# Performance work log

Measured on AMD Instinct MI355X. Metric: run time of the kernel, lower is better.

## Reference

```python
import jax, jax.numpy as jnp
import numpy as np

B, SEQ, NF = 16, 512, 32
E, HID, PRED = 128, 512, 96
N_FFT, HOP, TOPM = 64, 32, 32
W = SEQ // HOP + 1          # 17 windows (centered STFT)
F = N_FFT // 2 + 1          # 33 onesided freqs
LAM = 0.01                  # sparsity_threshold (softshrink)
SCALE = 0.02


def _hann(n):
    # periodic hann, matches torch.hann_window default
    return 0.5 - 0.5 * jnp.cos(2.0 * jnp.pi * jnp.arange(n) / n)


def _softshrink(v):
    return jnp.sign(v) * jnp.maximum(jnp.abs(v) - LAM, 0.0)


def setup_inputs():
    key = jax.random.key(0)
    ks = jax.random.split(key, 12)
    d = {}
    d['x'] = jax.random.normal(ks[0], (B, SEQ, NF), jnp.float32)
    d['embeddings'] = jax.random.normal(ks[1], (1, E), jnp.float32)
    for nm, k in zip(['Wr', 'Wi', 'Wrl', 'Wil', 'Wrr', 'Wir'], ks[2:8]):
        d[nm] = SCALE * jax.random.normal(k, (W, E, E), jnp.float32)
    d['br'] = SCALE * jax.random.normal(ks[8], (W, E), jnp.float32)
    d['bi'] = SCALE * jax.random.normal(ks[9], (W, E), jnp.float32)
    d['fc_w1'] = SCALE * jax.random.normal(ks[10], (SEQ * E, HID), jnp.float32)
    d['fc_b1'] = jnp.zeros((HID,), jnp.float32)
    d['fc_w2'] = SCALE * jax.random.normal(ks[11], (HID, PRED), jnp.float32)
    d['fc_b2'] = jnp.zeros((PRED,), jnp.float32)
    return d


def _forward(x, embeddings, Wr, Wi, Wrl, Wil, Wrr, Wir, br, bi,
             fc_w1, fc_b1, fc_w2, fc_b2):
    Bq, T, N = x.shape
    # tokenEmb: (B,T,N) -> (B,N,T,E)
    xe = x.transpose(0, 2, 1)[..., None] * embeddings
    bias = xe
    # ---- STFT (centered, reflect pad, hann, onesided) ----
    xt = xe.transpose(0, 1, 3, 2)                      # (B,N,E,T)
    pad = N_FFT // 2
    xp = jnp.pad(xt, ((0, 0), (0, 0), (0, 0), (pad, pad)), mode='reflect')
    win = _hann(N_FFT).astype(x.dtype)
    idx = jnp.arange(W)[:, None] * HOP + jnp.arange(N_FFT)[None, :]  # (W,nfft)
    frames = xp[..., idx] * win                        # (B,N,E,W,nfft)
    spec = jnp.fft.rfft(frames, axis=-1)               # (B,N,E,W,F)
    spec = spec.transpose(0, 1, 3, 4, 2)               # (B,N,W,F,E)
    # ---- top-M frequency select (dim=3) ----
    sm = jnp.moveaxis(spec, 3, -1)                     # (B,N,W,E,F)
    _, top_idx = jax.lax.top_k(jnp.abs(sm), TOPM)      # (B,N,W,E,M)
    vals = jnp.take_along_axis(sm, top_idx, axis=-1)
    xw = jnp.moveaxis(vals, -1, 3)                     # (B,N,W,M,E)
    # ---- per-window complex MLP with left/right neighbor windows ----
    z0 = jnp.zeros_like(xw[:, :, :1])
    xl = jnp.concatenate([z0, xw[:, :, :-1]], axis=2)  # left neighbor (zero at w=0)
    xr = jnp.concatenate([xw[:, :, 1:], z0], axis=2)   # right neighbor (zero at w=W-1)

    def cmul(z, wr, wi):
        re = jnp.einsum('bnwme,wef->bnwmf', z.real, wr) - jnp.einsum('bnwme,wef->bnwmf', z.imag, wi)
        im = jnp.einsum('bnwme,wef->bnwmf', z.imag, wr) + jnp.einsum('bnwme,wef->bnwmf', z.real, wi)
        return re, im

    re_m, im_m = cmul(xw, Wr, Wi)
    re_l, im_l = cmul(xl, Wrl, Wil)
    re_r, im_r = cmul(xr, Wrr, Wir)
    o_re = jax.nn.relu(re_m + re_l + re_r + br[None, None, :, None, :])
    o_im = jax.nn.relu(im_m + im_l + im_r + bi[None, None, :, None, :])
    y = _softshrink(o_re) + 1j * _softshrink(o_im)     # (B,N,W,M,E) complex
    # ---- scatter-pad back to full frequency grid ----
    ym = jnp.moveaxis(y, 3, -1)                        # (B,N,W,E,M)
    K = Bq * N * W * E
    flat_vals = ym.reshape(K, TOPM)
    flat_idx = top_idx.reshape(K, TOPM)
    full = jnp.zeros((K, F), ym.dtype).at[jnp.arange(K)[:, None], flat_idx].set(flat_vals)
    spec_full = jnp.moveaxis(full.reshape(Bq, N, W, E, F), -1, 3)  # (B,N,W,F,E)
    # ---- ISTFT (windowed OLA / window-squared envelope, centered trim) ----
    sf = spec_full.transpose(0, 1, 4, 2, 3)            # (B,N,E,W,F)
    fr = jnp.fft.irfft(sf, n=N_FFT, axis=-1) * win     # (B,N,E,W,nfft)
    L = (W - 1) * HOP + N_FFT
    ola = jnp.zeros((Bq, N, E, L), fr.dtype).at[..., idx].add(fr)
    env = jnp.zeros((L,), win.dtype).at[idx].add(win * win)
    ola = ola / jnp.where(env > 1e-11, env, 1.0)
    xt2 = ola[..., pad:L - pad]                        # (B,N,E,T)
    xo = xt2.transpose(0, 1, 3, 2) + bias              # (B,N,T,E) + residual
    # ---- fc head ----
    h = xo.reshape(Bq, N, T * E)
    h = jax.nn.leaky_relu(h @ fc_w1 + fc_b1, 0.01)
    out = h @ fc_w2 + fc_b2                            # (B,N,PRED)
    return out.transpose(0, 2, 1)                      # (B,PRED,N)


def reference(x, embeddings, Wr, Wi, Wrl, Wil, Wrr, Wir, br, bi,
              fc_w1, fc_b1, fc_w2, fc_b2):
    return _forward(x, embeddings, Wr, Wi, Wrl, Wil, Wrr, Wir, br, bi,
                    fc_w1, fc_b1, fc_w2, fc_b2)
```

## Files before the change

### kernel.cpp

```cpp
#include <hip/hip_runtime.h>
#include <hip/hip_bf16.h>

#define LAM 0.01f

typedef __attribute__((ext_vector_type(8))) short v8s;
typedef __attribute__((ext_vector_type(4))) float v4f;

static __device__ __forceinline__ unsigned short f2bf(float f) {
    union { float f; unsigned int u; } v; v.f = f;
    unsigned int u = v.u;
    u += 0x7fffu + ((u >> 16) & 1u);
    return (unsigned short)(u >> 16);
}
static __device__ __forceinline__ float bf2f(unsigned short h) {
    union { unsigned int u; float f; } c; c.u = ((unsigned int)h) << 16;
    return c.f;
}
static __device__ __forceinline__ unsigned int pkbf(float a, float b) {
    union { __hip_bfloat162 h; unsigned int u; } c;
    c.h = __float22bfloat162_rn(float2{a, b});
    return c.u;
}

static __device__ __forceinline__ void async16(const void* g, void* l) {
    __builtin_amdgcn_global_load_lds(
        (const __attribute__((address_space(1))) unsigned int*)g,
        (__attribute__((address_space(3))) unsigned int*)l, 16, 0, 0);
}

#define OFF_COEF 0ull
#define OFF_V    69632ull
#define OFF_BINS 2297856ull
#define OFF_AIMG 3411968ull
#define OFF_W1P  70520832ull
#define OFF_HP   137629696ull

__global__ __launch_bounds__(128) void coef_kernel(
    const float* __restrict__ emb,
    const float* __restrict__ Wr, const float* __restrict__ Wi,
    const float* __restrict__ Wrl, const float* __restrict__ Wil,
    const float* __restrict__ Wrr, const float* __restrict__ Wir,
    const float* __restrict__ br, const float* __restrict__ bi,
    float* __restrict__ coef)
{
    int w = blockIdx.x, j = blockIdx.y, e = threadIdx.x;
    float out;
    if (j < 6) {
        const float* Wj;
        switch (j) {
            case 0: Wj = Wr; break; case 1: Wj = Wi; break;
            case 2: Wj = Wrl; break; case 3: Wj = Wil; break;
            case 4: Wj = Wrr; break; default: Wj = Wir; break;
        }
        const float* p = Wj + (size_t)w * 16384 + e;
        float acc = 0.f;
        #pragma unroll 8
        for (int ep = 0; ep < 128; ++ep) acc = fmaf(emb[ep], p[ep * 128], acc);
        out = acc;
    } else if (j == 6) {
        out = br[w * 128 + e] - LAM;
    } else {
        out = bi[w * 128 + e] - LAM;
    }
    coef[((size_t)(w * 128 + e)) * 8 + j] = out;
}

__global__ __launch_bounds__(256) void stft_kernel(
    const float* __restrict__ x, float2* __restrict__ V, int* __restrict__ bins)
{
    __shared__ float sig[576];
    __shared__ float winT[64];
    __shared__ float2 tw[64];
    __shared__ float2 Sbuf[17 * 33];
    __shared__ float absb[17 * 33];

    const int blk = blockIdx.x;
    const int b = blk >> 5, n = blk & 31;
    const int tid = threadIdx.x;
    const float C64 = 0.09817477042468103f;

    if (tid < 64) {
        float ang = (float)tid * C64;
        winT[tid] = 0.5f - 0.5f * cosf(ang);
        tw[tid] = make_float2(cosf(ang), sinf(ang));
    }
    for (int l = tid; l < 576; l += 256) {
        int t = (l < 32) ? (32 - l) : ((l < 544) ? (l - 32) : (1054 - l));
        sig[l] = x[(size_t)b * 16384 + t * 32 + n];
    }
    __syncthreads();

    for (int task = tid; task < 561; task += 256) {
        int w = task / 33, f = task - w * 33;
        float sr = 0.f, si = 0.f;
        int base = w * 32;
        for (int t = 0; t < 64; ++t) {
            float sw = sig[base + t] * winT[t];
            float2 cs = tw[(f * t) & 63];
            sr = fmaf(sw, cs.x, sr);
            si = fmaf(sw, -cs.y, si);
        }
        Sbuf[task] = make_float2(sr, si);
        absb[task] = sqrtf(fmaf(sr, sr, si * si));
    }
    __syncthreads();

    for (int task = tid; task < 561; task += 256) {
        int w = task / 33, f = task - w * 33;
        float a = absb[task];
        int base = w * 33, rank = 0;
        for (int j = 0; j < 33; ++j) {
            float aj = absb[base + j];
            rank += (aj > a) || (aj == a && j < f);
        }
        if (rank < 32) {
            size_t o = ((size_t)blk * 17 + w) * 32 + rank;
            V[o] = Sbuf[task];
            bins[o] = f;
        }
    }
}

__global__ __launch_bounds__(256) void cvt_kernel(
    const float* __restrict__ w1, unsigned short* __restrict__ w1p)
{
    __shared__ float T[32][132];
    const int kb = blockIdx.x, nt = blockIdx.y;
    const int tid = threadIdx.x;

    #pragma unroll
    for (int p = 0; p < 4; ++p) {
        int r = (tid >> 5) + p * 8;
        int c = (tid & 31) * 4;
        float4 v = *(const float4*)&w1[((size_t)(kb * 32 + r)) * 512 + nt * 128 + c];
        T[r][c] = v.x; T[r][c + 1] = v.y; T[r][c + 2] = v.z; T[r][c + 3] = v.w;
    }
    __syncthreads();

    unsigned short* dst = w1p + ((size_t)nt * 2048 + kb) * 4096;
    #pragma unroll
    for (int p = 0; p < 2; ++p) {
        int pos = tid + 256 * p;
        int np = pos >> 2, cs = pos & 3;
        int clog = cs ^ ((np >> 2) & 3);
        unsigned int pk[4];
        #pragma unroll
        for (int j2 = 0; j2 < 4; ++j2)
            pk[j2] = pkbf(T[clog * 8 + j2 * 2][np], T[clog * 8 + j2 * 2 + 1][np]);
        *(uint4*)&dst[pos * 8] = make_uint4(pk[0], pk[1], pk[2], pk[3]);
    }
}

#define MID_ROLL(J0, J1, J2, J3)                                                \
    {                                                                           \
        _Pragma("unroll") for (int e2 = 0; e2 < 2; ++e2)                        \
        _Pragma("unroll") for (int i = 0; i < 4; ++i) {                         \
            roll[e2][J0][i] = fmaf(acc[0][e2][i], win16[0][i], roll[e2][J0][i]);\
            roll[e2][J1][i] = fmaf(acc[1][e2][i], win16[1][i], roll[e2][J1][i]);\
            roll[e2][J2][i] = fmaf(acc[2][e2][i], win16[2][i], roll[e2][J2][i]);\
            roll[e2][J3][i] = fmaf(acc[3][e2][i], win16[3][i], roll[e2][J3][i]);\
        }                                                                       \
    }

#define MID_FLUSH(JJA, JJB)                                                     \
    {                                                                           \
        _Pragma("unroll") for (int i = 0; i < 4; ++i) {                         \
            int tp = 32 * (w - 1) + q * 4 + i;                                  \
            float xb = xs[tp];                                                  \
            _Pragma("unroll") for (int e2 = 0; e2 < 2; ++e2) {                  \
                float val = fmaf(roll[e2][JJA][i], renv[0][i], xb * emb2[e2]);  \
                Aimg[cbase[e2] + (size_t)tp * 16384] = f2bf(val);               \
                roll[e2][JJA][i] = 0.f;                                         \
            }                                                                   \
            int tp2 = tp + 16;                                                  \
            float xb2 = xs[tp2];                                                \
            _Pragma("unroll") for (int e2 = 0; e2 < 2; ++e2) {                  \
                float val = fmaf(roll[e2][JJB][i], renv[1][i], xb2 * emb2[e2]); \
                Aimg[cbase[e2] + (size_t)tp2 * 16384] = f2bf(val);              \
                roll[e2][JJB][i] = 0.f;                                         \
            }                                                                   \
        }                                                                       \
    }

__global__ __launch_bounds__(256) void mid_kernel(
    const float* __restrict__ x, const float* __restrict__ emb,
    const float* __restrict__ coef, const float2* __restrict__ V,
    const int* __restrict__ bins, unsigned short* __restrict__ Aimg)
{
    __shared__ unsigned short M1t[2][64 * 72];
    __shared__ unsigned short Yt[2][128 * 72];
    __shared__ float cosT[64];
    __shared__ float sinT[64];
    __shared__ float2 Vs2[19 * 32];
    __shared__ int Bns[17 * 32];
    __shared__ float xs[512];

    const int blk = blockIdx.x;
    const int b = blk >> 5, n = blk & 31;
    const int tid = threadIdx.x;
    const int wave = tid >> 6, lane = tid & 63, l15 = lane & 15, q = lane >> 4;
    const float C64 = 0.09817477042468103f;

    if (tid < 64) {
        float ang = (float)tid * C64;
        cosT[tid] = __cosf(ang);
        sinT[tid] = __sinf(ang);
    }
    {
        const float2* Vg = V + (size_t)blk * 544;
        const int* Bg = bins + (size_t)blk * 544;
        for (int i = tid; i < 544; i += 256) { Vs2[32 + i] = Vg[i]; Bns[i] = Bg[i]; }
        if (tid < 64) {
            int r = (tid < 32) ? tid : (18 * 32 + tid - 32);
            Vs2[r] = make_float2(0.f, 0.f);
        }
        for (int i = tid; i < 512; i += 256) xs[i] = x[(size_t)b * 16384 + i * 32 + n];
    }

    float win16[4][4];
    #pragma unroll
    for (int tt = 0; tt < 4; ++tt)
        #pragma unroll
        for (int i = 0; i < 4; ++i) {
            int t = tt * 16 + q * 4 + i;
            win16[tt][i] = 0.5f - 0.5f * __cosf((float)t * C64);
        }
    float renv[2][4];
    #pragma unroll
    for (int hf = 0; hf < 2; ++hf)
        #pragma unroll
        for (int i = 0; i < 4; ++i) {
            int k = hf * 16 + q * 4 + i;
            float w0 = 0.5f - 0.5f * __cosf((float)k * C64);
            float w1v = 0.5f - 0.5f * __cosf((float)(k + 32) * C64);
            renv[hf][i] = 1.0f / (w0 * w0 + w1v * w1v);
        }
    int ebase[2];
    float emb2[2];
    size_t cbase[2];
    const int mt = blk >> 7, mp = blk & 127, s = (mp >> 2) & 3;
    #pragma unroll
    for (int e2 = 0; e2 < 2; ++e2) {
        ebase[e2] = (wave * 2 + e2) * 16 + l15;
        emb2[e2] = emb[ebase[e2]];
        int e = ebase[e2];
        int echunk = e >> 5, clog = (e >> 3) & 3, cs = clog ^ s, el = e & 7;
        cbase[e2] = ((size_t)mt * 2048 + echunk) * 4096 + mp * 32 + cs * 8 + el;
    }

    float roll[2][4][4];
    #pragma unroll
    for (int e2 = 0; e2 < 2; ++e2)
        #pragma unroll
        for (int jj = 0; jj < 4; ++jj)
            #pragma unroll
            for (int i = 0; i < 4; ++i) roll[e2][jj][i] = 0.f;

    const int e1 = tid & 127;
    const int mg = (tid >> 7) << 4;
    const int tM = tid & 63;
    const int kg = wave << 4;

    __syncthreads();

    for (int w = 0; w < 17; ++w) {
        const int buf = w & 1;
        {
            const float4* cf = (const float4*)(coef + ((size_t)(w * 128 + e1)) * 8);
            float4 cA = cf[0];
            float4 cB = cf[1];
            unsigned int rep[8], imp[8];
            #pragma unroll
            for (int j2 = 0; j2 < 8; ++j2) {
                float rev[2], imv[2];
                #pragma unroll
                for (int sdx = 0; sdx < 2; ++sdx) {
                    int m = mg + j2 * 2 + sdx;
                    float2 vm = Vs2[(w + 1) * 32 + m];
                    float2 vl = Vs2[w * 32 + m];
                    float2 vp = Vs2[(w + 2) * 32 + m];
                    float re = cB.z;
                    re = fmaf(vm.x, cA.x, re); re = fmaf(-vm.y, cA.y, re);
                    re = fmaf(vl.x, cA.z, re); re = fmaf(-vl.y, cA.w, re);
                    re = fmaf(vp.x, cB.x, re); re = fmaf(-vp.y, cB.y, re);
                    float im = cB.w;
                    im = fmaf(vm.y, cA.x, im); im = fmaf(vm.x, cA.y, im);
                    im = fmaf(vl.y, cA.z, im); im = fmaf(vl.x, cA.w, im);
                    im = fmaf(vp.y, cB.x, im); im = fmaf(vp.x, cB.y, im);
                    rev[sdx] = fmaxf(re, 0.f);
                    imv[sdx] = fmaxf(im, 0.f);
                }
                rep[j2] = pkbf(rev[0], rev[1]);
                imp[j2] = pkbf(imv[0], imv[1]);
            }
            uint4* dr = (uint4*)&Yt[buf][e1 * 72 + mg];
            dr[0] = make_uint4(rep[0], rep[1], rep[2], rep[3]);
            dr[1] = make_uint4(rep[4], rep[5], rep[6], rep[7]);
            uint4* di = (uint4*)&Yt[buf][e1 * 72 + 32 + mg];
            di[0] = make_uint4(imp[0], imp[1], imp[2], imp[3]);
            di[1] = make_uint4(imp[4], imp[5], imp[6], imp[7]);
        }
        {
            unsigned int mpk[8];
            #pragma unroll
            for (int j2 = 0; j2 < 8; ++j2) {
                float vv[2];
                #pragma unroll
                for (int sdx = 0; sdx < 2; ++sdx) {
                    int k = kg + j2 * 2 + sdx;
                    int m = k & 31;
                    int r = Bns[w * 32 + m];
                    float sc = (r == 0 || r == 32) ? 0.015625f : 0.03125f;
                    int idx = (r * tM) & 63;
                    vv[sdx] = (k < 32) ? (cosT[idx] * sc) : (-sinT[idx] * sc);
                }
                mpk[j2] = pkbf(vv[0], vv[1]);
            }
            uint4* dm = (uint4*)&M1t[buf][tM * 72 + kg];
            dm[0] = make_uint4(mpk[0], mpk[1], mpk[2], mpk[3]);
            dm[1] = make_uint4(mpk[4], mpk[5], mpk[6], mpk[7]);
        }
        __syncthreads();

        v4f acc[4][2];
        #pragma unroll
        for (int tt = 0; tt < 4; ++tt)
            #pragma unroll
            for (int e2 = 0; e2 < 2; ++e2) acc[tt][e2] = (v4f){0.f, 0.f, 0.f, 0.f};
        #pragma unroll
        for (int ks = 0; ks < 2; ++ks) {
            v8s bfr[2];
            #pragma unroll
            for (int e2 = 0; e2 < 2; ++e2)
                bfr[e2] = *(const v8s*)&Yt[buf][ebase[e2] * 72 + ks * 32 + q * 8];
            #pragma unroll
            for (int tt = 0; tt < 4; ++tt) {
                v8s af = *(const v8s*)&M1t[buf][(tt * 16 + l15) * 72 + ks * 32 + q * 8];
                #pragma unroll
                for (int e2 = 0; e2 < 2; ++e2)
                    acc[tt][e2] = __builtin_amdgcn_mfma_f32_16x16x32_bf16(
                        af, bfr[e2], acc[tt][e2], 0, 0, 0);
            }
        }

        if ((w & 1) == 0) {
            MID_ROLL(0, 1, 2, 3);
            if (w > 0) {
                MID_FLUSH(0, 1);
            } else {
                #pragma unroll
                for (int e2 = 0; e2 < 2; ++e2)
                    #pragma unroll
                    for (int i = 0; i < 4; ++i) {
                        roll[e2][0][i] = 0.f; roll[e2][1][i] = 0.f;
                    }
            }
        } else {
            MID_ROLL(2, 3, 0, 1);
            MID_FLUSH(2, 3);
        }
    }
}

__global__ __launch_bounds__(512) void gemm_kernel(
    const unsigned short* __restrict__ Aimg, const unsigned short* __restrict__ w1p,
    unsigned short* __restrict__ hp, int iters, int KS)
{
    __shared__ unsigned short As[2][8192];
    __shared__ unsigned short Bs[2][8192];

    const int gid = blockIdx.x;
    const int xcd = gid & 7;
    const int u = gid >> 3;
    const int KS4 = KS >> 2;
    const int nt2 = (u >= KS4) ? 1 : 0;
    const int vv = u - nt2 * KS4;
    const int pid = vv * 8 + xcd;
    const int ks = pid >> 1;
    const int mt2 = pid & 1;

    const int tid = threadIdx.x;
    const int wave = tid >> 6, lane = tid & 63;
    const int l15 = lane & 15, q = lane >> 4;
    const int kb0 = ks * iters;

    const int isB = wave >> 2;
    const int sub = wave & 3;
    const unsigned short* gsrc = (isB
        ? w1p + ((size_t)(nt2 * 2 + (sub >> 1)) * 2048 + kb0) * 4096
        : Aimg + ((size_t)(mt2 * 2 + (sub >> 1)) * 2048 + kb0) * 4096)
        + (sub & 1) * 2048 + lane * 8;
    const int ldsoff = (sub >> 1) * 4096 + (sub & 1) * 2048;

    v4f acc[4][8];
    #pragma unroll
    for (int mf = 0; mf < 4; ++mf)
        #pragma unroll
        for (int nf = 0; nf < 8; ++nf) acc[mf][nf] = (v4f){0.f, 0.f, 0.f, 0.f};

    {
        unsigned short* dst = (isB ? Bs[0] : As[0]) + ldsoff;
        #pragma unroll
        for (int j = 0; j < 4; ++j) async16(gsrc + j * 512, dst + j * 512);
    }

    const int wm = wave >> 1, wn = wave & 1;
    const int ca = (q ^ ((l15 >> 2) & 3)) * 8;
    const int rA = (wm >> 1) * 4096 + ((wm & 1) * 64 + l15) * 32 + ca;
    const int rB = wn * 4096 + l15 * 32 + ca;

    for (int it = 0; it < iters; ++it) {
        __syncthreads();
        if (it + 1 < iters) {
            const unsigned short* src = gsrc + (size_t)(it + 1) * 4096;
            unsigned short* dst = (isB ? Bs[(it + 1) & 1] : As[(it + 1) & 1]) + ldsoff;
            #pragma unroll
            for (int j = 0; j < 4; ++j) async16(src + j * 512, dst + j * 512);
        }
        const int cur = it & 1;
        v8s af[4], bf[8];
        #pragma unroll
        for (int f = 0; f < 4; ++f) af[f] = *(const v8s*)&As[cur][rA + f * 512];
        #pragma unroll
        for (int nf = 0; nf < 8; ++nf) bf[nf] = *(const v8s*)&Bs[cur][rB + nf * 512];
        #pragma unroll
        for (int mf = 0; mf < 4; ++mf)
            #pragma unroll
            for (int nf = 0; nf < 8; ++nf)
                acc[mf][nf] = __builtin_amdgcn_mfma_f32_16x16x32_bf16(
                    af[mf], bf[nf], acc[mf][nf], 0, 0, 0);
    }

    #pragma unroll
    for (int mf = 0; mf < 4; ++mf)
        #pragma unroll
        for (int nf = 0; nf < 8; ++nf) {
            int row = mt2 * 256 + wm * 64 + mf * 16 + q * 4;
            int col = nt2 * 256 + wn * 128 + nf * 16 + l15;
            unsigned short* dst = hp + ((size_t)row * KS + ks) * 512 + col;
            #pragma unroll
            for (int i = 0; i < 4; ++i)
                dst[(size_t)i * KS * 512] = f2bf(acc[mf][nf][i]);
        }
}

__global__ __launch_bounds__(256) void fc2_kernel(
    const unsigned short* __restrict__ hp, const float* __restrict__ b1,
    const float* __restrict__ w2, const float* __restrict__ b2,
    float* __restrict__ out, int KS)
{
    __shared__ float hbuf[512];
    const int row = blockIdx.x;
    const int tid = threadIdx.x;

    const unsigned int* base = (const unsigned int*)(hp + (size_t)row * KS * 512) + tid;
    float a0 = 0.f, a1 = 0.f;
    #pragma unroll 8
    for (int k = 0; k < KS; ++k) {
        unsigned int v = base[k * 256];
        a0 += bf2f((unsigned short)(v & 0xffff));
        a1 += bf2f((unsigned short)(v >> 16));
    }
    float s0 = a0 + b1[tid * 2];
    float s1 = a1 + b1[tid * 2 + 1];
    hbuf[tid * 2]     = (s0 > 0.f) ? s0 : 0.01f * s0;
    hbuf[tid * 2 + 1] = (s1 > 0.f) ? s1 : 0.01f * s1;
    __syncthreads();

    if (tid < 96) {
        float a = b2[tid];
        #pragma unroll 8
        for (int h = 0; h < 512; ++h) a = fmaf(hbuf[h], w2[h * 96 + tid], a);
        int b = row >> 5, n = row & 31;
        out[(size_t)b * 3072 + tid * 32 + n] = a;
    }
}

extern "C" void kernel_launch(void* const* d_in, const int* in_sizes, int n_in,
                              void* d_out, int out_size, void* d_ws, size_t ws_size,
                              hipStream_t stream) {
    const float* x   = (const float*)d_in[0];
    const float* emb = (const float*)d_in[1];
    const float* Wr  = (const float*)d_in[2];
    const float* Wi  = (const float*)d_in[3];
    const float* Wrl = (const float*)d_in[4];
    const float* Wil = (const float*)d_in[5];
    const float* Wrr = (const float*)d_in[6];
    const float* Wir = (const float*)d_in[7];
    const float* br  = (const float*)d_in[8];
    const float* bi  = (const float*)d_in[9];
    const float* w1  = (const float*)d_in[10];
    const float* b1  = (const float*)d_in[11];
    const float* w2  = (const float*)d_in[12];
    const float* b2  = (const float*)d_in[13];

    char* ws = (char*)d_ws;
    float* coef          = (float*)(ws + OFF_COEF);
    float2* V            = (float2*)(ws + OFF_V);
    int* bins            = (int*)(ws + OFF_BINS);
    unsigned short* Aimg = (unsigned short*)(ws + OFF_AIMG);
    unsigned short* w1p  = (unsigned short*)(ws + OFF_W1P);
    unsigned short* hpp  = (unsigned short*)(ws + OFF_HP);

    int KS = 64;
    size_t hp_bytes = (size_t)KS * 512 * 512 * 2;
    if (OFF_HP + hp_bytes > ws_size) {
        KS = 32; hp_bytes = (size_t)KS * 512 * 512 * 2;
    }
    int iters = 2048 / KS;

    coef_kernel<<<dim3(17, 8), dim3(128), 0, stream>>>(
        emb, Wr, Wi, Wrl, Wil, Wrr, Wir, br, bi, coef);
    cvt_kernel<<<dim3(2048, 4), dim3(256), 0, stream>>>(w1, w1p);
    stft_kernel<<<dim3(512), dim3(256), 0, stream>>>(x, V, bins);
    mid_kernel<<<dim3(512), dim3(256), 0, stream>>>(x, emb, coef, V, bins, Aimg);
    gemm_kernel<<<dim3(4 * KS), dim3(512), 0, stream>>>(Aimg, w1p, hpp, iters, KS);
    fc2_kernel<<<dim3(512), dim3(256), 0, stream>>>(hpp, b1, w2, b2, (float*)d_out, KS);
}
```

Measured before the change: 405.1 us.

## Fuse prep kernels, merge STFT into mid, triple-buffer GEMM, split fc2 reduction

Folds the coefficient kernel into the weight-conversion kernel as an extra grid row, and merges the STFT/top-k kernel into the mid kernel so spectra and bins stay in shared memory instead of going through global memory. The GEMM moves from double to triple buffering with explicit vmcnt waits, so loads run two stages ahead. fc2 splits its hidden-dimension dot product across two thread groups. The aim is fewer launches, less global traffic and better load/compute overlap, at the cost of more LDS per block, which can lower occupancy.

```diff
diff --git a/kernel.cpp b/kernel.cpp
--- a/kernel.cpp
+++ b/kernel.cpp
@@ -29,13 +29,12 @@
 }
 
 #define OFF_COEF 0ull
-#define OFF_V    69632ull
-#define OFF_BINS 2297856ull
 #define OFF_AIMG 3411968ull
 #define OFF_W1P  70520832ull
 #define OFF_HP   137629696ull
 
-__global__ __launch_bounds__(128) void coef_kernel(
+__global__ __launch_bounds__(256) void pre_kernel(
+    const float* __restrict__ w1, unsigned short* __restrict__ w1p,
     const float* __restrict__ emb,
     const float* __restrict__ Wr, const float* __restrict__ Wi,
     const float* __restrict__ Wrl, const float* __restrict__ Wil,
@@ -43,31 +42,101 @@
     const float* __restrict__ br, const float* __restrict__ bi,
     float* __restrict__ coef)
 {
-    int w = blockIdx.x, j = blockIdx.y, e = threadIdx.x;
-    float out;
-    if (j < 6) {
-        const float* Wj;
-        switch (j) {
-            case 0: Wj = Wr; break; case 1: Wj = Wi; break;
-            case 2: Wj = Wrl; break; case 3: Wj = Wil; break;
-            case 4: Wj = Wrr; break; default: Wj = Wir; break;
-        }
-        const float* p = Wj + (size_t)w * 16384 + e;
-        float acc = 0.f;
-        #pragma unroll 8
-        for (int ep = 0; ep < 128; ++ep) acc = fmaf(emb[ep], p[ep * 128], acc);
-        out = acc;
-    } else if (j == 6) {
-        out = br[w * 128 + e] - LAM;
-    } else {
-        out = bi[w * 128 + e] - LAM;
-    }
-    coef[((size_t)(w * 128 + e)) * 8 + j] = out;
-}
-
-__global__ __launch_bounds__(256) void stft_kernel(
-    const float* __restrict__ x, float2* __restrict__ V, int* __restrict__ bins)
+    if (blockIdx.y == 4) {
+        const int bx = blockIdx.x;
+        if (bx >= 68) return;
+        const int pair = bx * 2 + (threadIdx.x >> 7);
+        const int w = pair >> 3, j = pair & 7, e = threadIdx.x & 127;
+        float out;
+        if (j < 6) {
+            const float* Wj;
+            switch (j) {
+                case 0: Wj = Wr; break; case 1: Wj = Wi; break;
+                case 2: Wj = Wrl; break; case 3: Wj = Wil; break;
+                case 4: Wj = Wrr; break; default: Wj = Wir; break;
+            }
+            const float* p = Wj + (size_t)w * 16384 + e;
+            float acc = 0.f;
+            #pragma unroll 8
+            for (int ep = 0; ep < 128; ++ep) acc = fmaf(emb[ep], p[ep * 128], acc);
+            out = acc;
+        } else if (j == 6) {
+            out = br[w * 128 + e] - LAM;
+        } else {
+            out = bi[w * 128 + e] - LAM;
+        }
+        coef[((size_t)(w * 128 + e)) * 8 + j] = out;
+        return;
+    }
+
+    __shared__ float T[32][132];
+    const int kb = blockIdx.x, nt = blockIdx.y;
+    const int tid = threadIdx.x;
+
+    #pragma unroll
+    for (int p = 0; p < 4; ++p) {
+        int r = (tid >> 5) + p * 8;
+        int c = (tid & 31) * 4;
+        float4 v = *(const float4*)&w1[((size_t)(kb * 32 + r)) * 512 + nt * 128 + c];
+        T[r][c] = v.x; T[r][c + 1] = v.y; T[r][c + 2] = v.z; T[r][c + 3] = v.w;
+    }
+    __syncthreads();
+
+    unsigned short* dst = w1p + ((size_t)nt * 2048 + kb) * 4096;
+    #pragma unroll
+    for (int p = 0; p < 2; ++p) {
+        int pos = tid + 256 * p;
+        int np = pos >> 2, cs = pos & 3;
+        int clog = cs ^ ((np >> 2) & 3);
+        unsigned int pk[4];
+        #pragma unroll
+        for (int j2 = 0; j2 < 4; ++j2)
+            pk[j2] = pkbf(T[clog * 8 + j2 * 2][np], T[clog * 8 + j2 * 2 + 1][np]);
+        *(uint4*)&dst[pos * 8] = make_uint4(pk[0], pk[1], pk[2], pk[3]);
+    }
+}
+
+#define MID_ROLL(J0, J1, J2, J3)                                                \
+    {                                                                           \
+        _Pragma("unroll") for (int e2 = 0; e2 < 2; ++e2)                        \
+        _Pragma("unroll") for (int i = 0; i < 4; ++i) {                         \
+            roll[e2][J0][i] = fmaf(acc[0][e2][i], win16[0][i], roll[e2][J0][i]);\
+            roll[e2][J1][i] = fmaf(acc[1][e2][i], win16[1][i], roll[e2][J1][i]);\
+            roll[e2][J2][i] = fmaf(acc[2][e2][i], win16[2][i], roll[e2][J2][i]);\
+            roll[e2][J3][i] = fmaf(acc[3][e2][i], win16[3][i], roll[e2][J3][i]);\
+        }                                                                       \
+    }
+
+#define MID_FLUSH(JJA, JJB)                                                     \
+    {                                                                           \
+        _Pragma("unroll") for (int i = 0; i < 4; ++i) {                         \
+            int tp = 32 * (w - 1) + q * 4 + i;                                  \
+            float xb = sig[tp + 32];                                            \
+            _Pragma("unroll") for (int e2 = 0; e2 < 2; ++e2) {                  \
+                float val = fmaf(roll[e2][JJA][i], renv[0][i], xb * emb2[e2]);  \
+                Aimg[cbase[e2] + (size_t)tp * 16384] = f2bf(val);               \
+                roll[e2][JJA][i] = 0.f;                                         \
+            }                                                                   \
+            int tp2 = tp + 16;                                                  \
+            float xb2 = sig[tp2 + 32];                                          \
+            _Pragma("unroll") for (int e2 = 0; e2 < 2; ++e2) {                  \
+                float val = fmaf(roll[e2][JJB][i], renv[1][i], xb2 * emb2[e2]); \
+                Aimg[cbase[e2] + (size_t)tp2 * 16384] = f2bf(val);              \
+                roll[e2][JJB][i] = 0.f;                                         \
+            }                                                                   \
+        }                                                                       \
+    }
+
+__global__ __launch_bounds__(256) void stftmid_kernel(
+    const float* __restrict__ x, const float* __restrict__ emb,
+    const float* __restrict__ coef, unsigned short* __restrict__ Aimg)
 {
+    __shared__ unsigned short M1t[2][64 * 72];
+    __shared__ unsigned short Yt[2][128 * 72];
+    __shared__ float cosT[64];
+    __shared__ float sinT[64];
+    __shared__ float2 Vs2[19 * 32];
+    __shared__ int Bns[17 * 32];
     __shared__ float sig[576];
     __shared__ float winT[64];
     __shared__ float2 tw[64];
@@ -77,12 +146,17 @@
     const int blk = blockIdx.x;
     const int b = blk >> 5, n = blk & 31;
     const int tid = threadIdx.x;
+    const int wave = tid >> 6, lane = tid & 63, l15 = lane & 15, q = lane >> 4;
     const float C64 = 0.09817477042468103f;
 
     if (tid < 64) {
         float ang = (float)tid * C64;
         winT[tid] = 0.5f - 0.5f * cosf(ang);
         tw[tid] = make_float2(cosf(ang), sinf(ang));
+        cosT[tid] = __cosf(ang);
+        sinT[tid] = __sinf(ang);
+        int r = (tid < 32) ? tid : (18 * 32 + tid - 32);
+        Vs2[r] = make_float2(0.f, 0.f);
     }
     for (int l = tid; l < 576; l += 256) {
         int t = (l < 32) ? (32 - l) : ((l < 544) ? (l - 32) : (1054 - l));
@@ -114,107 +188,9 @@
             rank += (aj > a) || (aj == a && j < f);
         }
         if (rank < 32) {
-            size_t o = ((size_t)blk * 17 + w) * 32 + rank;
-            V[o] = Sbuf[task];
-            bins[o] = f;
-        }
-    }
-}
-
-__global__ __launch_bounds__(256) void cvt_kernel(
-    const float* __restrict__ w1, unsigned short* __restrict__ w1p)
-{
-    __shared__ float T[32][132];
-    const int kb = blockIdx.x, nt = blockIdx.y;
-    const int tid = threadIdx.x;
-
-    #pragma unroll
-    for (int p = 0; p < 4; ++p) {
-        int r = (tid >> 5) + p * 8;
-        int c = (tid & 31) * 4;
-        float4 v = *(const float4*)&w1[((size_t)(kb * 32 + r)) * 512 + nt * 128 + c];
-        T[r][c] = v.x; T[r][c + 1] = v.y; T[r][c + 2] = v.z; T[r][c + 3] = v.w;
-    }
-    __syncthreads();
-
-    unsigned short* dst = w1p + ((size_t)nt * 2048 + kb) * 4096;
-    #pragma unroll
-    for (int p = 0; p < 2; ++p) {
-        int pos = tid + 256 * p;
-        int np = pos >> 2, cs = pos & 3;
-        int clog = cs ^ ((np >> 2) & 3);
-        unsigned int pk[4];
-        #pragma unroll
-        for (int j2 = 0; j2 < 4; ++j2)
-            pk[j2] = pkbf(T[clog * 8 + j2 * 2][np], T[clog * 8 + j2 * 2 + 1][np]);
-        *(uint4*)&dst[pos * 8] = make_uint4(pk[0], pk[1], pk[2], pk[3]);
-    }
-}
-
-#define MID_ROLL(J0, J1, J2, J3)                                                \
-    {                                                                           \
-        _Pragma("unroll") for (int e2 = 0; e2 < 2; ++e2)                        \
-        _Pragma("unroll") for (int i = 0; i < 4; ++i) {                         \
-            roll[e2][J0][i] = fmaf(acc[0][e2][i], win16[0][i], roll[e2][J0][i]);\
-            roll[e2][J1][i] = fmaf(acc[1][e2][i], win16[1][i], roll[e2][J1][i]);\
-            roll[e2][J2][i] = fmaf(acc[2][e2][i], win16[2][i], roll[e2][J2][i]);\
-            roll[e2][J3][i] = fmaf(acc[3][e2][i], win16[3][i], roll[e2][J3][i]);\
-        }                                                                       \
-    }
-
-#define MID_FLUSH(JJA, JJB)                                                     \
-    {                                                                           \
-        _Pragma("unroll") for (int i = 0; i < 4; ++i) {                         \
-            int tp = 32 * (w - 1) + q * 4 + i;                                  \
-            float xb = xs[tp];                                                  \
-            _Pragma("unroll") for (int e2 = 0; e2 < 2; ++e2) {                  \
-                float val = fmaf(roll[e2][JJA][i], renv[0][i], xb * emb2[e2]);  \
-                Aimg[cbase[e2] + (size_t)tp * 16384] = f2bf(val);               \
-                roll[e2][JJA][i] = 0.f;                                         \
-            }                                                                   \
-            int tp2 = tp + 16;                                                  \
-            float xb2 = xs[tp2];                                                \
-            _Pragma("unroll") for (int e2 = 0; e2 < 2; ++e2) {                  \
-                float val = fmaf(roll[e2][JJB][i], renv[1][i], xb2 * emb2[e2]); \
-                Aimg[cbase[e2] + (size_t)tp2 * 16384] = f2bf(val);              \
-                roll[e2][JJB][i] = 0.f;                                         \
-            }                                                                   \
-        }                                                                       \
-    }
-
-__global__ __launch_bounds__(256) void mid_kernel(
-    const float* __restrict__ x, const float* __restrict__ emb,
-    const float* __restrict__ coef, const float2* __restrict__ V,
-    const int* __restrict__ bins, unsigned short* __restrict__ Aimg)
-{
-    __shared__ unsigned short M1t[2][64 * 72];
-    __shared__ unsigned short Yt[2][128 * 72];
-    __shared__ float cosT[64];
-    __shared__ float sinT[64];
-    __shared__ float2 Vs2[19 * 32];
-    __shared__ int Bns[17 * 32];
-    __shared__ float xs[512];
-
-    const int blk = blockIdx.x;
-    const int b = blk >> 5, n = blk & 31;
-    const int tid = threadIdx.x;
-    const int wave = tid >> 6, lane = tid & 63, l15 = lane & 15, q = lane >> 4;
-    const float C64 = 0.09817477042468103f;
-
-    if (tid < 64) {
-        float ang = (float)tid * C64;
-        cosT[tid] = __cosf(ang);
-        sinT[tid] = __sinf(ang);
-    }
-    {
-        const float2* Vg = V + (size_t)blk * 544;
-        const int* Bg = bins + (size_t)blk * 544;
-        for (int i = tid; i < 544; i += 256) { Vs2[32 + i] = Vg[i]; Bns[i] = Bg[i]; }
-        if (tid < 64) {
-            int r = (tid < 32) ? tid : (18 * 32 + tid - 32);
-            Vs2[r] = make_float2(0.f, 0.f);
-        }
-        for (int i = tid; i < 512; i += 256) xs[i] = x[(size_t)b * 16384 + i * 32 + n];
+            Vs2[32 + w * 32 + rank] = Sbuf[task];
+            Bns[w * 32 + rank] = f;
+        }
     }
 
     float win16[4][4];
@@ -366,8 +342,8 @@
     const unsigned short* __restrict__ Aimg, const unsigned short* __restrict__ w1p,
     unsigned short* __restrict__ hp, int iters, int KS)
 {
-    __shared__ unsigned short As[2][8192];
-    __shared__ unsigned short Bs[2][8192];
+    __shared__ unsigned short As[3][8192];
+    __shared__ unsigned short Bs[3][8192];
 
     const int gid = blockIdx.x;
     const int xcd = gid & 7;
@@ -399,9 +375,15 @@
         for (int nf = 0; nf < 8; ++nf) acc[mf][nf] = (v4f){0.f, 0.f, 0.f, 0.f};
 
     {
-        unsigned short* dst = (isB ? Bs[0] : As[0]) + ldsoff;
-        #pragma unroll
-        for (int j = 0; j < 4; ++j) async16(gsrc + j * 512, dst + j * 512);
+        unsigned short* dst0 = (isB ? Bs[0] : As[0]) + ldsoff;
+        #pragma unroll
+        for (int j = 0; j < 4; ++j) async16(gsrc + j * 512, dst0 + j * 512);
+        if (iters > 1) {
+            const unsigned short* s1 = gsrc + 4096;
+            unsigned short* dst1 = (isB ? Bs[1] : As[1]) + ldsoff;
+            #pragma unroll
+            for (int j = 0; j < 4; ++j) async16(s1 + j * 512, dst1 + j * 512);
+        }
     }
 
     const int wm = wave >> 1, wn = wave & 1;
@@ -410,14 +392,21 @@
     const int rB = wn * 4096 + l15 * 32 + ca;
 
     for (int it = 0; it < iters; ++it) {
-        __syncthreads();
         if (it + 1 < iters) {
-            const unsigned short* src = gsrc + (size_t)(it + 1) * 4096;
-            unsigned short* dst = (isB ? Bs[(it + 1) & 1] : As[(it + 1) & 1]) + ldsoff;
+            asm volatile("s_waitcnt vmcnt(4)" ::: "memory");
+        } else {
+            asm volatile("s_waitcnt vmcnt(0)" ::: "memory");
+        }
+        __builtin_amdgcn_s_barrier();
+        __builtin_amdgcn_sched_barrier(0);
+        if (it + 2 < iters) {
+            const int nb = (it + 2) % 3;
+            const unsigned short* src = gsrc + (size_t)(it + 2) * 4096;
+            unsigned short* dst = (isB ? Bs[nb] : As[nb]) + ldsoff;
             #pragma unroll
             for (int j = 0; j < 4; ++j) async16(src + j * 512, dst + j * 512);
         }
-        const int cur = it & 1;
+        const int cur = it % 3;
         v8s af[4], bf[8];
         #pragma unroll
         for (int f = 0; f < 4; ++f) af[f] = *(const v8s*)&As[cur][rA + f * 512];
@@ -450,6 +439,7 @@
     float* __restrict__ out, int KS)
 {
     __shared__ float hbuf[512];
+    __shared__ float part[2][96];
     const int row = blockIdx.x;
     const int tid = threadIdx.x;
 
@@ -467,10 +457,19 @@
     hbuf[tid * 2 + 1] = (s1 > 0.f) ? s1 : 0.01f * s1;
     __syncthreads();
 
+    if (tid < 192) {
+        const int c = (tid >= 96) ? 1 : 0;
+        const int o = tid - 96 * c;
+        float a = 0.f;
+        #pragma unroll 8
+        for (int h = c * 256; h < c * 256 + 256; ++h)
+            a = fmaf(hbuf[h], w2[h * 96 + o], a);
+        part[c][o] = a;
+    }
+    __syncthreads();
+
     if (tid < 96) {
-        float a = b2[tid];
-        #pragma unroll 8
-        for (int h = 0; h < 512; ++h) a = fmaf(hbuf[h], w2[h * 96 + tid], a);
+        float a = part[0][tid] + part[1][tid] + b2[tid];
         int b = row >> 5, n = row & 31;
         out[(size_t)b * 3072 + tid * 32 + n] = a;
     }
@@ -496,8 +495,6 @@
 
     char* ws = (char*)d_ws;
     float* coef          = (float*)(ws + OFF_COEF);
-    float2* V            = (float2*)(ws + OFF_V);
-    int* bins            = (int*)(ws + OFF_BINS);
     unsigned short* Aimg = (unsigned short*)(ws + OFF_AIMG);
     unsigned short* w1p  = (unsigned short*)(ws + OFF_W1P);
     unsigned short* hpp  = (unsigned short*)(ws + OFF_HP);
@@ -509,11 +506,9 @@
     }
     int iters = 2048 / KS;
 
-    coef_kernel<<<dim3(17, 8), dim3(128), 0, stream>>>(
-        emb, Wr, Wi, Wrl, Wil, Wrr, Wir, br, bi, coef);
-    cvt_kernel<<<dim3(2048, 4), dim3(256), 0, stream>>>(w1, w1p);
-    stft_kernel<<<dim3(512), dim3(256), 0, stream>>>(x, V, bins);
-    mid_kernel<<<dim3(512), dim3(256), 0, stream>>>(x, emb, coef, V, bins, Aimg);
+    pre_kernel<<<dim3(2048, 5), dim3(256), 0, stream>>>(
+        w1, w1p, emb, Wr, Wi, Wrl, Wil, Wrr, Wir, br, bi, coef);
+    stftmid_kernel<<<dim3(512), dim3(256), 0, stream>>>(x, emb, coef, Aimg);
     gemm_kernel<<<dim3(4 * KS), dim3(512), 0, stream>>>(Aimg, w1p, hpp, iters, KS);
     fc2_kernel<<<dim3(512), dim3(256), 0, stream>>>(hpp, b1, w2, b2, (float*)d_out, KS);
 }
```

Measured after the change: 435.2 us. 1.07x slower.
